# Optimization experiments

Hardware: AMD Instinct MI355X
Metric: run time of the kernel (lower is better)

The kernel has to match this reference:

```python
import jax, jax.numpy as jnp
import numpy as np

N_NODES = 100000
NEG_SLOPE = 0.2  # DGL GATConv default


def gat_layer(x, W, al, ar, src, dst):
    # x: [N, F_in], W: [F_in, H*D], al/ar: [H, D]
    H, D = al.shape
    f = (x @ W).reshape(-1, H, D)                      # [N, H, D]
    el = jnp.einsum('nhd,hd->nh', f, al)               # src attn term
    er = jnp.einsum('nhd,hd->nh', f, ar)               # dst attn term
    e = jax.nn.leaky_relu(el[src] + er[dst], NEG_SLOPE)  # [E, H]
    # segment softmax over incoming edges of each dst node
    m = jax.ops.segment_max(e, dst, num_segments=N_NODES)
    m = jnp.where(jnp.isfinite(m), m, jnp.zeros_like(m))  # isolated nodes -> -inf guard
    ex = jnp.exp(e - m[dst])                           # [E, H]
    s = jax.ops.segment_sum(ex, dst, num_segments=N_NODES)
    alpha = ex / (s[dst] + 1e-9)                       # [E, H]
    msg = f[src] * alpha[:, :, None]                   # [E, H, D]
    out = jax.ops.segment_sum(msg, dst, num_segments=N_NODES)  # [N, H, D]
    return out.reshape(N_NODES, H * D)


def setup_inputs() -> dict:
    key = jax.random.key(0)
    ks = jax.random.split(key, 12)
    x = jax.random.normal(ks[0], (N_NODES, 128), dtype=jnp.float32)
    edge_index = jax.random.randint(ks[1], (2, 1600000), 0, N_NODES, dtype=jnp.int32)
    sc = 0.05
    W0 = jax.random.normal(ks[2], (128, 128), dtype=jnp.float32) * sc
    al0 = jax.random.normal(ks[3], (4, 32), dtype=jnp.float32) * sc
    ar0 = jax.random.normal(ks[4], (4, 32), dtype=jnp.float32) * sc
    W1 = jax.random.normal(ks[5], (128, 128), dtype=jnp.float32) * sc
    al1 = jax.random.normal(ks[6], (4, 32), dtype=jnp.float32) * sc
    ar1 = jax.random.normal(ks[7], (4, 32), dtype=jnp.float32) * sc
    W2 = jax.random.normal(ks[8], (128, 128), dtype=jnp.float32) * sc
    al2 = jax.random.normal(ks[9], (4, 32), dtype=jnp.float32) * sc
    ar2 = jax.random.normal(ks[10], (4, 32), dtype=jnp.float32) * sc
    return {"x": x, "edge_index": edge_index,
            "W0": W0, "al0": al0, "ar0": ar0,
            "W1": W1, "al1": al1, "ar1": ar1,
            "W2": W2, "al2": al2, "ar2": ar2}


def reference(x, edge_index, W0, al0, ar0, W1, al1, ar1, W2, al2, ar2):
    src, dst = edge_index[0], edge_index[1]
    h = x
    for (W, al, ar) in ((W0, al0, ar0), (W1, al1, ar1), (W2, al2, ar2)):
        h = gat_layer(h, W, al, ar, src, dst)
        h = jax.nn.relu(h)  # dropout_rate = 0.0 -> identity
    return h
```

## Files before the change

kernel.cpp:

```cpp
#include <hip/hip_runtime.h>
#include <math.h>

#define NEG_SLOPE 0.2f
#define NBUCK 512
#define BHCHUNK 8192
#define BCHUNK 4096
#define ESLICE 4

typedef __attribute__((ext_vector_type(8))) short short8;
typedef __attribute__((ext_vector_type(4))) float f32x4;

__device__ __forceinline__ unsigned short bf16rne(float x) {
    unsigned u = __float_as_uint(x);
    u += 0x7fffu + ((u >> 16) & 1u);
    return (unsigned short)(u >> 16);
}
__device__ __forceinline__ unsigned pack_bf2(float x, float y) {
    unsigned ux = __float_as_uint(x), uy = __float_as_uint(y);
    ux = (ux + 0x7fffu + ((ux >> 16) & 1u)) >> 16;
    uy = (uy + 0x7fffu + ((uy >> 16) & 1u)) & 0xffff0000u;
    return ux | uy;
}

__global__ __launch_bounds__(256) void k_front(
    const int* __restrict__ dst, int* __restrict__ bcnt, int E,
    const float4* __restrict__ x, uint4* __restrict__ Xb, int n8,
    const float* __restrict__ w0, const float* __restrict__ w1,
    const float* __restrict__ w2, unsigned short* __restrict__ Wt,
    int nbB, int nbCvt) {
    __shared__ int cnt[NBUCK];
    int bb = blockIdx.x, t = threadIdx.x;
    if (bb < nbB) {
        for (int i = t; i < NBUCK; i += 256) cnt[i] = 0;
        __syncthreads();
        int e0 = bb * BHCHUNK;
        int n = min(BHCHUNK, E - e0);
        for (int i = t; i < n; i += 256) atomicAdd(&cnt[dst[e0 + i] >> 8], 1);
        __syncthreads();
        for (int i = t; i < NBUCK; i += 256)
            if (cnt[i]) atomicAdd(&bcnt[i], cnt[i]);
    } else if (bb < nbB + nbCvt) {
        int id = (bb - nbB) * 256 + t;
        if (id < n8) {
            float4 a = x[id * 2], b = x[id * 2 + 1];
            uint4 o;
            o.x = pack_bf2(a.x, a.y);
            o.y = pack_bf2(a.z, a.w);
            o.z = pack_bf2(b.x, b.y);
            o.w = pack_bf2(b.z, b.w);
            Xb[id] = o;
        }
    } else {
        int id = (bb - nbB - nbCvt) * 256 + t;
        int layer = id >> 14, rem = id & 16383;
        int k = rem >> 7, n = rem & 127;
        const float* W = (layer == 0) ? w0 : (layer == 1) ? w1 : w2;
        Wt[layer * 16384 + n * 128 + k] = bf16rne(W[k * 128 + n]);
    }
}

__global__ void k_bscan(const int* __restrict__ bcnt, int* __restrict__ bbase,
                        int* __restrict__ bcur, int* __restrict__ rowstart,
                        int N, int E) {
    __shared__ int sd[NBUCK];
    int t = threadIdx.x;
    int c = bcnt[t];
    sd[t] = c;
    __syncthreads();
    for (int s = 1; s < NBUCK; s <<= 1) {
        int x = (t >= s) ? sd[t - s] : 0;
        __syncthreads();
        sd[t] += x;
        __syncthreads();
    }
    int excl = sd[t] - c;
    bbase[t] = excl;
    bcur[t] = excl;
    if (t == NBUCK - 1) bbase[NBUCK] = excl + c;
    if (t == 0) rowstart[N] = E;
}

__global__ __launch_bounds__(256) void k_bin(
    const int* __restrict__ src, const int* __restrict__ dst,
    int* __restrict__ bcur, unsigned* __restrict__ packed, int E) {
    __shared__ int cnt[NBUCK];
    __shared__ int gbase[NBUCK];
    for (int i = threadIdx.x; i < NBUCK; i += 256) cnt[i] = 0;
    __syncthreads();
    int e0 = blockIdx.x * BCHUNK;
    int n = min(BCHUNK, E - e0);
    for (int i = threadIdx.x; i < n; i += 256)
        atomicAdd(&cnt[dst[e0 + i] >> 8], 1);
    __syncthreads();
    for (int i = threadIdx.x; i < NBUCK; i += 256) {
        int c = cnt[i];
        gbase[i] = c ? atomicAdd(&bcur[i], c) : 0;
        cnt[i] = 0;
    }
    __syncthreads();
    for (int i = threadIdx.x; i < n; i += 256) {
        int d = dst[e0 + i];
        int b = d >> 8;
        int o = atomicAdd(&cnt[b], 1);
        packed[gbase[b] + o] = ((unsigned)src[e0 + i] << 8) | (unsigned)(d & 255);
    }
}

__global__ __launch_bounds__(256) void k_place2(
    const unsigned* __restrict__ packed, const int* __restrict__ bbase,
    int* __restrict__ rowstart, unsigned* __restrict__ cpack, int N) {
    __shared__ int cnt[256], sd[256], lcur[256];
    int b = blockIdx.x, t = threadIdx.x;
    int base = bbase[b], end = bbase[b + 1];
    cnt[t] = 0;
    __syncthreads();
    for (int i = base + t; i < end; i += 256)
        atomicAdd(&cnt[packed[i] & 255u], 1);
    __syncthreads();
    sd[t] = cnt[t];
    __syncthreads();
    for (int s = 1; s < 256; s <<= 1) {
        int x = (t >= s) ? sd[t - s] : 0;
        __syncthreads();
        sd[t] += x;
        __syncthreads();
    }
    int excl = sd[t] - cnt[t];
    int gid = (b << 8) + t;
    if (gid < N) rowstart[gid] = base + excl;
    lcur[t] = base + excl;
    __syncthreads();
    for (int i = base + t; i < end; i += 256) {
        unsigned p = packed[i];
        unsigned dl = p & 255u;
        int pos = atomicAdd(&lcur[dl], 1);
        cpack[pos] = (dl << 17) | (p >> 8);
    }
}

__global__ __launch_bounds__(256) void k_gemm(
    const unsigned short* __restrict__ Ab,
    const unsigned short* __restrict__ Wt,
    const float* __restrict__ alv, const float* __restrict__ arv,
    unsigned short* __restrict__ Fb,
    float* __restrict__ el, float* __restrict__ er, int M) {
    __shared__ unsigned short cst[4][32][128];
    int t = threadIdx.x;
    int wv = t >> 6, l = t & 63;
    int l15 = l & 15, quad = l >> 4;
    int row0 = blockIdx.x * 128 + wv * 32;

    f32x4 acc[2][8];
#pragma unroll
    for (int mi = 0; mi < 2; mi++)
#pragma unroll
        for (int nt = 0; nt < 8; nt++)
            acc[mi][nt] = (f32x4){0.f, 0.f, 0.f, 0.f};

    int rA0 = min(row0 + l15, M - 1);
    int rA1 = min(row0 + 16 + l15, M - 1);
    const uint4* pA0 = (const uint4*)(Ab + (size_t)rA0 * 128) + quad;
    const uint4* pA1 = (const uint4*)(Ab + (size_t)rA1 * 128) + quad;
    const uint4* pW = (const uint4*)Wt;

#pragma unroll
    for (int ks = 0; ks < 4; ks++) {
        union { uint4 u; short8 s; } a0, a1, b[8];
        a0.u = pA0[ks * 4];
        a1.u = pA1[ks * 4];
#pragma unroll
        for (int nt = 0; nt < 8; nt++)
            b[nt].u = pW[(nt * 16 + l15) * 16 + quad + ks * 4];
#pragma unroll
        for (int nt = 0; nt < 8; nt++) {
            acc[0][nt] = __builtin_amdgcn_mfma_f32_16x16x32_bf16(a0.s, b[nt].s, acc[0][nt], 0, 0, 0);
            acc[1][nt] = __builtin_amdgcn_mfma_f32_16x16x32_bf16(a1.s, b[nt].s, acc[1][nt], 0, 0, 0);
        }
    }

#pragma unroll
    for (int mi = 0; mi < 2; mi++)
#pragma unroll
        for (int nt = 0; nt < 8; nt++)
#pragma unroll
            for (int r = 0; r < 4; r++)
                cst[wv][mi * 16 + quad * 4 + r][nt * 16 + l15] = bf16rne(acc[mi][nt][r]);

    int rrow = l >> 1;
    int cb = (l & 1) * 64;
    int grow = row0 + rrow;
    bool ok = grow < M;
    float pe[2] = {0.f, 0.f}, pr[2] = {0.f, 0.f};
#pragma unroll
    for (int i = 0; i < 8; i++) {
        uint4 v = *(const uint4*)&cst[wv][rrow][cb + i * 8];
        if (ok) ((uint4*)(Fb + (size_t)grow * 128 + cb))[i] = v;
        int hi = i >> 2;
        int c0 = cb + i * 8;
        unsigned uu[4] = {v.x, v.y, v.z, v.w};
#pragma unroll
        for (int q = 0; q < 4; q++) {
            float fa = __uint_as_float(uu[q] << 16);
            float fb = __uint_as_float(uu[q] & 0xffff0000u);
            pe[hi] += fa * alv[c0 + 2 * q] + fb * alv[c0 + 2 * q + 1];
            pr[hi] += fa * arv[c0 + 2 * q] + fb * arv[c0 + 2 * q + 1];
        }
    }
    float qe0 = __shfl_xor(pe[0], 1, 64), qe1 = __shfl_xor(pe[1], 1, 64);
    float qr0 = __shfl_xor(pr[0], 1, 64), qr1 = __shfl_xor(pr[1], 1, 64);
    if (((l & 1) == 0) && ok) {
        *(float4*)&el[(size_t)grow * 4] = make_float4(pe[0], pe[1], qe0, qe1);
        *(float4*)&er[(size_t)grow * 4] = make_float4(pr[0], pr[1], qr0, qr1);
    }
}

__global__ __launch_bounds__(256) void k_edge(
    const unsigned* __restrict__ cpack, const int* __restrict__ bbase,
    const float4* __restrict__ el4, const float4* __restrict__ er4,
    float4* __restrict__ pw4) {
    int b = blockIdx.x >> 2;
    int slice = blockIdx.x & (ESLICE - 1);
    int t = slice * 256 + threadIdx.x;
    int base = bbase[b], end = bbase[b + 1];
    for (int i = base + t; i < end; i += 256 * ESLICE) {
        unsigned w = cpack[i];
        int s = (int)(w & 0x1ffffu);
        int d = (b << 8) + (int)(w >> 17);
        float4 l = el4[s], r = er4[d];
        float4 o;
        float e;
        e = l.x + r.x; e = fmaxf(e, NEG_SLOPE * e); o.x = __expf(e);
        e = l.y + r.y; e = fmaxf(e, NEG_SLOPE * e); o.y = __expf(e);
        e = l.z + r.z; e = fmaxf(e, NEG_SLOPE * e); o.z = __expf(e);
        e = l.w + r.w; e = fmaxf(e, NEG_SLOPE * e); o.w = __expf(e);
        pw4[i] = o;
    }
}

template <int OUT_BF16>
__global__ __launch_bounds__(256) void k_aggr(
    const int* __restrict__ rowstart, const unsigned* __restrict__ cpack,
    const float* __restrict__ pw, const uint4* __restrict__ F4,
    void* __restrict__ outp, int N, int E) {
    int lane = threadIdx.x & 63;
    int sub = lane >> 4;
    int l16 = lane & 15;
    int w = blockIdx.x * 16 + ((threadIdx.x >> 6) << 2) + sub;
    bool active = w < N;
    int wc = active ? w : N - 1;
    int start = rowstart[wc];
    int dg = active ? (rowstart[wc + 1] - start) : 0;
    int h = l16 >> 2;

    float s_acc = 0.f;
    float a0 = 0.f, a1 = 0.f, a2 = 0.f, a3 = 0.f;
    float a4 = 0.f, a5 = 0.f, a6 = 0.f, a7 = 0.f;

    int ncc = (dg + 3) >> 2;
    int m = max(ncc, __shfl_xor(ncc, 16, 64));
    int nccmax = max(m, __shfl_xor(m, 32, 64));
    int full = dg >> 2;
    int mf = min(full, __shfl_xor(full, 16, 64));
    int minfull = min(mf, __shfl_xor(mf, 32, 64));

    auto loadc = [&](int c, uint4* fb, float* pb) {
        int j = c << 2;
        if (c < minfull) {
#pragma unroll
            for (int u = 0; u < 4; u++) {
                int e = start + j + u;
                int s = (int)(cpack[e] & 0x1ffffu);
                fb[u] = F4[(size_t)s * 16 + l16];
                pb[u] = pw[(size_t)e * 4 + h];
            }
        } else {
#pragma unroll
            for (int u = 0; u < 4; u++) {
                int jj = j + u;
                int e = min(max(start + min(jj, dg - 1), 0), E - 1);
                int s = (int)(cpack[e] & 0x1ffffu);
                fb[u] = F4[(size_t)s * 16 + l16];
                float pv = pw[(size_t)e * 4 + h];
                pb[u] = (jj < dg) ? pv : 0.f;
            }
        }
    };
    auto consume = [&](const uint4* fb, const float* pb) {
#pragma unroll
        for (int u = 0; u < 4; u++) {
            float p = pb[u];
            s_acc += p;
            a0 += p * __uint_as_float(fb[u].x << 16);
            a1 += p * __uint_as_float(fb[u].x & 0xffff0000u);
            a2 += p * __uint_as_float(fb[u].y << 16);
            a3 += p * __uint_as_float(fb[u].y & 0xffff0000u);
            a4 += p * __uint_as_float(fb[u].z << 16);
            a5 += p * __uint_as_float(fb[u].z & 0xffff0000u);
            a6 += p * __uint_as_float(fb[u].w << 16);
            a7 += p * __uint_as_float(fb[u].w & 0xffff0000u);
        }
    };

    uint4 f0[4], f1[4];
    float p0[4], p1[4];
    if (nccmax > 0) {
        loadc(0, f0, p0);
        for (int c = 1; c < nccmax; c++) {
            if (c & 1) { loadc(c, f1, p1); consume(f0, p0); }
            else       { loadc(c, f0, p0); consume(f1, p1); }
        }
        if (nccmax & 1) consume(f0, p0); else consume(f1, p1);
    }

    if (!active) return;
    float inv = 1.f / (s_acc + 1e-9f);
    a0 = fmaxf(a0 * inv, 0.f); a1 = fmaxf(a1 * inv, 0.f);
    a2 = fmaxf(a2 * inv, 0.f); a3 = fmaxf(a3 * inv, 0.f);
    a4 = fmaxf(a4 * inv, 0.f); a5 = fmaxf(a5 * inv, 0.f);
    a6 = fmaxf(a6 * inv, 0.f); a7 = fmaxf(a7 * inv, 0.f);
    if (OUT_BF16) {
        uint4 pk;
        pk.x = pack_bf2(a0, a1);
        pk.y = pack_bf2(a2, a3);
        pk.z = pack_bf2(a4, a5);
        pk.w = pack_bf2(a6, a7);
        ((uint4*)outp)[(size_t)w * 16 + l16] = pk;
    } else {
        float4* op = (float4*)outp + (size_t)w * 32 + l16 * 2;
        op[0] = make_float4(a0, a1, a2, a3);
        op[1] = make_float4(a4, a5, a6, a7);
    }
}


extern "C" void kernel_launch(void* const* d_in, const int* in_sizes, int n_in,
                              void* d_out, int out_size, void* d_ws, size_t ws_size,
                              hipStream_t stream) {
    const float* x = (const float*)d_in[0];
    const int* ei = (const int*)d_in[1];
    int N = in_sizes[0] / 128;
    int E = in_sizes[1] / 2;
    const int* src = ei;
    const int* dst = ei + E;
    const float* Wm[3] = {(const float*)d_in[2], (const float*)d_in[5], (const float*)d_in[8]};
    const float* al[3] = {(const float*)d_in[3], (const float*)d_in[6], (const float*)d_in[9]};
    const float* ar[3] = {(const float*)d_in[4], (const float*)d_in[7], (const float*)d_in[10]};

    char* p = (char*)d_ws;
    auto carve = [&](size_t bytes) {
        char* r = p;
        p += (bytes + 255) & ~(size_t)255;
        return r;
    };
    unsigned short* Xb = (unsigned short*)carve((size_t)N * 128 * 2);
    unsigned short* Hb = (unsigned short*)carve((size_t)N * 128 * 2);
    unsigned short* Fb = (unsigned short*)carve((size_t)N * 128 * 2);
    unsigned short* Wt = (unsigned short*)carve((size_t)3 * 16384 * 2);
    float* el       = (float*)carve((size_t)N * 4 * 4);
    float* er       = (float*)carve((size_t)N * 4 * 4);
    float* pw       = (float*)carve((size_t)E * 4 * 4);
    int* rowstart   = (int*)carve((size_t)(N + 1) * 4);
    unsigned* cpack = (unsigned*)carve((size_t)E * 4);
    unsigned* packed= (unsigned*)carve((size_t)E * 4);
    int* bcnt       = (int*)carve((size_t)NBUCK * 4);
    int* bbase      = (int*)carve((size_t)(NBUCK + 1) * 4);
    int* bcur       = (int*)carve((size_t)NBUCK * 4);

    int NBUSED = (N + 255) >> 8;

    hipMemsetAsync(bcnt, 0, NBUCK * 4, stream);
    int nbB = (E + BHCHUNK - 1) / BHCHUNK;
    int n8 = N * 128 / 8;
    int nbCvt = (n8 + 255) / 256;
    int nbPrep = (3 * 16384) / 256;
    k_front<<<nbB + nbCvt + nbPrep, 256, 0, stream>>>(
        dst, bcnt, E, (const float4*)x, (uint4*)Xb, n8,
        Wm[0], Wm[1], Wm[2], Wt, nbB, nbCvt);
    k_bscan<<<1, NBUCK, 0, stream>>>(bcnt, bbase, bcur, rowstart, N, E);
    k_bin<<<(E + BCHUNK - 1) / BCHUNK, 256, 0, stream>>>(src, dst, bcur, packed, E);
    k_place2<<<NBUSED, 256, 0, stream>>>(packed, bbase, rowstart, cpack, N);

    int gb = (N + 127) / 128;
    int ab = (N + 15) / 16;
    k_gemm<<<gb, 256, 0, stream>>>(Xb, Wt, al[0], ar[0], Fb, el, er, N);
    k_edge<<<NBUSED * ESLICE, 256, 0, stream>>>(cpack, bbase, (const float4*)el,
                                                (const float4*)er, (float4*)pw);
    k_aggr<1><<<ab, 256, 0, stream>>>(rowstart, cpack, pw, (const uint4*)Fb, Hb, N, E);

    k_gemm<<<gb, 256, 0, stream>>>(Hb, Wt + 16384, al[1], ar[1], Fb, el, er, N);
    k_edge<<<NBUSED * ESLICE, 256, 0, stream>>>(cpack, bbase, (const float4*)el,
                                                (const float4*)er, (float4*)pw);
    k_aggr<1><<<ab, 256, 0, stream>>>(rowstart, cpack, pw, (const uint4*)Fb, Hb, N, E);

    k_gemm<<<gb, 256, 0, stream>>>(Hb, Wt + 32768, al[2], ar[2], Fb, el, er, N);
    k_edge<<<NBUSED * ESLICE, 256, 0, stream>>>(cpack, bbase, (const float4*)el,
                                                (const float4*)er, (float4*)pw);
    k_aggr<0><<<ab, 256, 0, stream>>>(rowstart, cpack, pw, (const uint4*)Fb, d_out, N, E);
}
```

Before: 526.4 us.

## Fuse edge attention scoring into aggregation kernel and drop edge-weight buffer

Removes the separate per-edge kernel that computed exp(leaky_relu(el[src]+er[dst])) into a 1.6M x 4 float buffer. The aggregation kernel now loads el for each source node and er once per destination, and computes the weight inline. This drops a write and a read of the edge-weight array plus three kernel launches per forward pass. In exchange, each edge's exp is recomputed by every lane in its head group (4 lanes), and there is an extra random gather of el per edge. Padded slots now use a large negative score so their exponentiated weight is zero.

```diff
diff --git a/kernel.cpp b/kernel.cpp
--- a/kernel.cpp
+++ b/kernel.cpp
@@ -5,7 +5,6 @@
 #define NBUCK 512
 #define BHCHUNK 8192
 #define BCHUNK 4096
-#define ESLICE 4
 
 typedef __attribute__((ext_vector_type(8))) short short8;
 typedef __attribute__((ext_vector_type(4))) float f32x4;
@@ -214,34 +213,11 @@
     }
 }
 
-__global__ __launch_bounds__(256) void k_edge(
-    const unsigned* __restrict__ cpack, const int* __restrict__ bbase,
-    const float4* __restrict__ el4, const float4* __restrict__ er4,
-    float4* __restrict__ pw4) {
-    int b = blockIdx.x >> 2;
-    int slice = blockIdx.x & (ESLICE - 1);
-    int t = slice * 256 + threadIdx.x;
-    int base = bbase[b], end = bbase[b + 1];
-    for (int i = base + t; i < end; i += 256 * ESLICE) {
-        unsigned w = cpack[i];
-        int s = (int)(w & 0x1ffffu);
-        int d = (b << 8) + (int)(w >> 17);
-        float4 l = el4[s], r = er4[d];
-        float4 o;
-        float e;
-        e = l.x + r.x; e = fmaxf(e, NEG_SLOPE * e); o.x = __expf(e);
-        e = l.y + r.y; e = fmaxf(e, NEG_SLOPE * e); o.y = __expf(e);
-        e = l.z + r.z; e = fmaxf(e, NEG_SLOPE * e); o.z = __expf(e);
-        e = l.w + r.w; e = fmaxf(e, NEG_SLOPE * e); o.w = __expf(e);
-        pw4[i] = o;
-    }
-}
-
 template <int OUT_BF16>
 __global__ __launch_bounds__(256) void k_aggr(
     const int* __restrict__ rowstart, const unsigned* __restrict__ cpack,
-    const float* __restrict__ pw, const uint4* __restrict__ F4,
-    void* __restrict__ outp, int N, int E) {
+    const float* __restrict__ el, const float* __restrict__ er,
+    const uint4* __restrict__ F4, void* __restrict__ outp, int N, int E) {
     int lane = threadIdx.x & 63;
     int sub = lane >> 4;
     int l16 = lane & 15;
@@ -251,6 +227,7 @@
     int start = rowstart[wc];
     int dg = active ? (rowstart[wc + 1] - start) : 0;
     int h = l16 >> 2;
+    float rr = er[(size_t)wc * 4 + h];
 
     float s_acc = 0.f;
     float a0 = 0.f, a1 = 0.f, a2 = 0.f, a3 = 0.f;
@@ -263,7 +240,7 @@
     int mf = min(full, __shfl_xor(full, 16, 64));
     int minfull = min(mf, __shfl_xor(mf, 32, 64));
 
-    auto loadc = [&](int c, uint4* fb, float* pb) {
+    auto loadc = [&](int c, uint4* fb, float* eb) {
         int j = c << 2;
         if (c < minfull) {
 #pragma unroll
@@ -271,7 +248,7 @@
                 int e = start + j + u;
                 int s = (int)(cpack[e] & 0x1ffffu);
                 fb[u] = F4[(size_t)s * 16 + l16];
-                pb[u] = pw[(size_t)e * 4 + h];
+                eb[u] = el[(size_t)s * 4 + h];
             }
         } else {
 #pragma unroll
@@ -280,15 +257,17 @@
                 int e = min(max(start + min(jj, dg - 1), 0), E - 1);
                 int s = (int)(cpack[e] & 0x1ffffu);
                 fb[u] = F4[(size_t)s * 16 + l16];
-                float pv = pw[(size_t)e * 4 + h];
-                pb[u] = (jj < dg) ? pv : 0.f;
+                float ev = el[(size_t)s * 4 + h];
+                eb[u] = (jj < dg) ? ev : -1e30f;
             }
         }
     };
-    auto consume = [&](const uint4* fb, const float* pb) {
+    auto consume = [&](const uint4* fb, const float* eb) {
 #pragma unroll
         for (int u = 0; u < 4; u++) {
-            float p = pb[u];
+            float e = eb[u] + rr;
+            e = fmaxf(e, NEG_SLOPE * e);
+            float p = __expf(e);
             s_acc += p;
             a0 += p * __uint_as_float(fb[u].x << 16);
             a1 += p * __uint_as_float(fb[u].x & 0xffff0000u);
@@ -302,14 +281,14 @@
     };
 
     uint4 f0[4], f1[4];
-    float p0[4], p1[4];
+    float e0[4], e1[4];
     if (nccmax > 0) {
-        loadc(0, f0, p0);
+        loadc(0, f0, e0);
         for (int c = 1; c < nccmax; c++) {
-            if (c & 1) { loadc(c, f1, p1); consume(f0, p0); }
-            else       { loadc(c, f0, p0); consume(f1, p1); }
-        }
-        if (nccmax & 1) consume(f0, p0); else consume(f1, p1);
+            if (c & 1) { loadc(c, f1, e1); consume(f0, e0); }
+            else       { loadc(c, f0, e0); consume(f1, e1); }
+        }
+        if (nccmax & 1) consume(f0, e0); else consume(f1, e1);
     }
 
     if (!active) return;
@@ -358,7 +337,6 @@
     unsigned short* Wt = (unsigned short*)carve((size_t)3 * 16384 * 2);
     float* el       = (float*)carve((size_t)N * 4 * 4);
     float* er       = (float*)carve((size_t)N * 4 * 4);
-    float* pw       = (float*)carve((size_t)E * 4 * 4);
     int* rowstart   = (int*)carve((size_t)(N + 1) * 4);
     unsigned* cpack = (unsigned*)carve((size_t)E * 4);
     unsigned* packed= (unsigned*)carve((size_t)E * 4);
@@ -383,17 +361,11 @@
     int gb = (N + 127) / 128;
     int ab = (N + 15) / 16;
     k_gemm<<<gb, 256, 0, stream>>>(Xb, Wt, al[0], ar[0], Fb, el, er, N);
-    k_edge<<<NBUSED * ESLICE, 256, 0, stream>>>(cpack, bbase, (const float4*)el,
-                                                (const float4*)er, (float4*)pw);
-    k_aggr<1><<<ab, 256, 0, stream>>>(rowstart, cpack, pw, (const uint4*)Fb, Hb, N, E);
+    k_aggr<1><<<ab, 256, 0, stream>>>(rowstart, cpack, el, er, (const uint4*)Fb, Hb, N, E);
 
     k_gemm<<<gb, 256, 0, stream>>>(Hb, Wt + 16384, al[1], ar[1], Fb, el, er, N);
-    k_edge<<<NBUSED * ESLICE, 256, 0, stream>>>(cpack, bbase, (const float4*)el,
-                                                (const float4*)er, (float4*)pw);
-    k_aggr<1><<<ab, 256, 0, stream>>>(rowstart, cpack, pw, (const uint4*)Fb, Hb, N, E);
+    k_aggr<1><<<ab, 256, 0, stream>>>(rowstart, cpack, el, er, (const uint4*)Fb, Hb, N, E);
 
     k_gemm<<<gb, 256, 0, stream>>>(Hb, Wt + 32768, al[2], ar[2], Fb, el, er, N);
-    k_edge<<<NBUSED * ESLICE, 256, 0, stream>>>(cpack, bbase, (const float4*)el,
-                                                (const float4*)er, (float4*)pw);
-    k_aggr<0><<<ab, 256, 0, stream>>>(rowstart, cpack, pw, (const uint4*)Fb, d_out, N, E);
-}
+    k_aggr<0><<<ab, 256, 0, stream>>>(rowstart, cpack, el, er, (const uint4*)Fb, d_out, N, E);
+}
```

After: 503.8 us. 1.04x faster.
